# Kernel optimization log

Hardware: AMD Instinct MI355X
Metric: run time of the kernel (lower is better)

## Reference

```python
import jax, jax.numpy as jnp
import numpy as np

B, S, E, H = 2, 2048, 1024, 16
D = E // H  # head_dim = 64
EPS = 1e-6


def _angle_decay():
    # angle: 1/10000**linspace(0,1,D//2), each value repeated twice (interleaved)
    a = 1.0 / (10000.0 ** jnp.linspace(0.0, 1.0, D // 2))
    angle = jnp.repeat(a, 2)  # [D]
    decay = jnp.log(1.0 - 2.0 ** (-5.0 - jnp.arange(H, dtype=jnp.float32)))  # [H]
    return angle, decay


def _rel_pos(slen):
    angle, decay = _angle_decay()
    idx = jnp.arange(slen, dtype=jnp.float32)
    sin = jnp.sin(idx[:, None] * angle[None, :])  # [S, D]
    cos = jnp.cos(idx[:, None] * angle[None, :])  # [S, D]
    diff = idx[:, None] - idx[None, :]            # [S, S]
    tril = diff >= 0
    masked = jnp.where(tril, diff, jnp.inf)
    mask = jnp.exp(masked * decay[:, None, None])  # [H, S, S]; exp(-inf)=0 on upper tri
    mask = jnp.nan_to_num(mask)
    mask = mask / jnp.sqrt(jnp.sum(mask, axis=-1, keepdims=True))
    return sin, cos, mask


def _rotate_every_two(x):
    x1 = x[..., ::2]
    x2 = x[..., 1::2]
    return jnp.stack((-x2, x1), axis=-1).reshape(x.shape)


def _theta_shift(x, sin, cos):
    # x: [B, H, S, D]; sin/cos: [S, D] broadcast over B,H
    return x * cos + _rotate_every_two(x) * sin


def setup_inputs() -> dict:
    key = jax.random.key(0)
    ks = jax.random.split(key, 5)
    scale = 1.0 / np.sqrt(E)
    return {
        "x": jax.random.normal(ks[0], (B, S, E), dtype=jnp.float32),
        "Wq": jax.random.normal(ks[1], (E, E), dtype=jnp.float32) * scale,
        "Wk": jax.random.normal(ks[2], (E, E), dtype=jnp.float32) * scale,
        "Wv": jax.random.normal(ks[3], (E, E), dtype=jnp.float32) * scale,
        "Wg": jax.random.normal(ks[4], (E, E), dtype=jnp.float32) * scale,
    }


def reference(x, Wq, Wk, Wv, Wg):
    bsz, tgt_len, _ = x.shape
    sin, cos, mask = _rel_pos(tgt_len)
    scaling = E ** (-0.5)

    q = x @ Wq
    k = (x @ Wk) * scaling
    v = x @ Wv
    g = x @ Wg

    q = q.reshape(bsz, tgt_len, H, D).transpose(0, 2, 1, 3)  # [B,H,S,D]
    k = k.reshape(bsz, tgt_len, H, D).transpose(0, 2, 1, 3)
    vr = v.reshape(bsz, tgt_len, H, D).transpose(0, 2, 1, 3)

    qr = _theta_shift(q, sin, cos)
    kr = _theta_shift(k, sin, cos)

    qk = jnp.einsum("bhqd,bhkd->bhqk", qr, kr) * mask[None]
    denom = jax.lax.stop_gradient(
        jnp.clip(jnp.sum(jnp.abs(qk), axis=-1, keepdims=True), 1.0, 5e4)
    )
    out = jnp.einsum("bhqk,bhkd->bhqd", qk / denom, vr)
    out = out.transpose(0, 2, 1, 3)  # [B,S,H,D]

    # RMSNorm over head_dim (no affine)
    out = out * jax.lax.rsqrt(jnp.mean(out * out, axis=-1, keepdims=True) + EPS)
    out = out.reshape(bsz, tgt_len, E)
    return jax.nn.silu(g) * out
```

## Files before the change

### kernel.cpp

```cpp
#include <hip/hip_runtime.h>

typedef unsigned short u16;
typedef unsigned int u32;
typedef __attribute__((ext_vector_type(8))) __bf16 bf16x8;
typedef __attribute__((ext_vector_type(4))) float f32x4;

#define B_SZ   2
#define S_LEN  2048
#define E_DIM  1024
#define NHEAD  16
#define HD     64
#define KDIM   1024
#define NQKV   3072

__device__ __forceinline__ float bf2f(u16 u){
  union { u32 i; float f; } c; c.i = ((u32)u) << 16; return c.f;
}
__device__ __forceinline__ u16 f2bf(float f){
  union { float f; u32 i; } c; c.f = f;
  return (u16)((c.i + 0x7FFFu + ((c.i >> 16) & 1u)) >> 16);
}
__device__ __forceinline__ u16 f2bf_fast(float f){
  union { float f; u32 i; } c; c.f = f;
  return (u16)((c.i + 0x8000u) >> 16);
}
__device__ __forceinline__ void gl2lds16(const void* g, void* l){
  __builtin_amdgcn_global_load_lds((const __attribute__((address_space(1))) void*)g,
                                   (__attribute__((address_space(3))) void*)l, 16, 0, 0);
}

__global__ __launch_bounds__(256) void castx_kernel(const float* __restrict__ x, u16* __restrict__ xb){
  size_t flat = ((size_t)blockIdx.x * 256 + threadIdx.x) * 16;
  int m7 = (int)((flat >> 10) & 7);
  int cb = (int)((flat >> 3) & 7);
  size_t tile = flat & ~(size_t)63;
  float f[16];
  #pragma unroll
  for (int c = 0; c < 4; c++) *(float4*)&f[c * 4] = *(const float4*)&x[flat + c * 4];
  u16 o[16];
  #pragma unroll
  for (int i = 0; i < 16; i++) o[i] = f2bf(f[i]);
  *(uint4*)&xb[tile + ((cb ^ m7) * 8)]       = *(uint4*)&o[0];
  *(uint4*)&xb[tile + (((cb + 1) ^ m7) * 8)] = *(uint4*)&o[8];
}

__global__ __launch_bounds__(256) void wtrans_kernel(const float* __restrict__ Wq, const float* __restrict__ Wk,
                                                     const float* __restrict__ Wv, const float* __restrict__ Wg,
                                                     u16* __restrict__ WT){
  const float* Ws[4] = {Wq, Wk, Wv, Wg};
  const float* W = Ws[blockIdx.z];
  int n0 = blockIdx.x * 64, k0 = blockIdx.y * 64;
  __shared__ u16 tile[64][66];
  int t = threadIdx.x;
  int r = t >> 2, cg = (t & 3) * 16;
  const float* src = W + (size_t)(k0 + r) * E_DIM + n0 + cg;
  float f[16];
  #pragma unroll
  for (int c = 0; c < 4; c++) *(float4*)&f[c * 4] = *(const float4*)&src[c * 4];
  #pragma unroll
  for (int i = 0; i < 16; i++) tile[r][cg + i] = f2bf(f[i]);
  __syncthreads();
  u16 ov[16];
  #pragma unroll
  for (int i = 0; i < 16; i++) ov[i] = tile[cg + i][r];
  int n7 = r & 7, cb = cg >> 3;
  u16* dst = WT + (size_t)(blockIdx.z * E_DIM + n0 + r) * KDIM + k0;
  *(uint4*)&dst[(cb ^ n7) * 8]       = *(uint4*)&ov[0];
  *(uint4*)&dst[((cb + 1) ^ n7) * 8] = *(uint4*)&ov[8];
}

__global__ __launch_bounds__(256) void gemm_kernel(const u16* __restrict__ A, const u16* __restrict__ Bt,
                                                   u16* __restrict__ qkv, u16* __restrict__ gc){
  __shared__ __align__(16) u16 As[128 * 64];
  __shared__ __align__(16) u16 Bs[128 * 64];
  int m0 = blockIdx.y * 128, n0 = blockIdx.x * 128;
  int t = threadIdx.x;
  int wave = t >> 6, lane = t & 63;
  int l15 = lane & 15, quad = lane >> 4, h8 = lane & 7;
  int r0 = (wave & 1) * 64, c0 = (wave >> 1) * 64;
  f32x4 acc[4][4];
  #pragma unroll
  for (int i = 0; i < 4; i++)
    #pragma unroll
    for (int j = 0; j < 4; j++) acc[i][j] = (f32x4){0.f, 0.f, 0.f, 0.f};

  for (int k0 = 0; k0 < KDIM; k0 += 64){
    __syncthreads();
    #pragma unroll
    for (int c = 0; c < 4; c++){
      int L = c * 256 + t;
      gl2lds16(A + (size_t)(m0 + (L >> 3)) * KDIM + k0 + (L & 7) * 8, &As[L * 8]);
    }
    #pragma unroll
    for (int c = 0; c < 4; c++){
      int L = c * 256 + t;
      gl2lds16(Bt + (size_t)(n0 + (L >> 3)) * KDIM + k0 + (L & 7) * 8, &Bs[L * 8]);
    }
    __syncthreads();
    #pragma unroll
    for (int kk = 0; kk < 2; kk++){
      bf16x8 a[4], b[4];
      #pragma unroll
      for (int i = 0; i < 4; i++) a[i] = *(const bf16x8*)&As[(r0 + i * 16 + l15) * 64 + ((kk * 4 + quad) ^ h8) * 8];
      #pragma unroll
      for (int j = 0; j < 4; j++) b[j] = *(const bf16x8*)&Bs[(c0 + j * 16 + l15) * 64 + ((kk * 4 + quad) ^ h8) * 8];
      #pragma unroll
      for (int i = 0; i < 4; i++)
        #pragma unroll
        for (int j = 0; j < 4; j++)
          acc[i][j] = __builtin_amdgcn_mfma_f32_16x16x32_bf16(a[i], b[j], acc[i][j], 0, 0, 0);
    }
  }
  if (n0 < 3072){
    #pragma unroll
    for (int i = 0; i < 4; i++){
      int row = m0 + r0 + i * 16 + quad * 4;
      #pragma unroll
      for (int j = 0; j < 4; j++){
        int col = n0 + c0 + j * 16 + l15;
        #pragma unroll
        for (int r = 0; r < 4; r++)
          qkv[(size_t)(row + r) * NQKV + col] = f2bf(acc[i][j][r]);
      }
    }
  } else {
    #pragma unroll
    for (int i = 0; i < 4; i++){
      int row = m0 + r0 + i * 16 + quad * 4;
      #pragma unroll
      for (int j = 0; j < 4; j++){
        int e = (n0 - 3072) + c0 + j * 16 + l15;
        #pragma unroll
        for (int r = 0; r < 4; r++)
          gc[(size_t)(row + r) * E_DIM + e] = f2bf(acc[i][j][r]);
      }
    }
  }
}

__global__ __launch_bounds__(256) void shift_kernel(const u16* __restrict__ qkv,
                                                    u16* __restrict__ qr, u16* __restrict__ kr,
                                                    u16* __restrict__ vt){
  int sb = blockIdx.x, bh = blockIdx.y;
  int s0 = sb * 64;
  int t = threadIdx.x;
  int sl = t >> 2, dg = (t & 3) * 16;
  int s = s0 + sl;
  int h = bh & 15;
  size_t token = (size_t)(bh >> 4) * S_LEN + s;
  size_t base = token * NQKV + h * HD + dg;
  u16 qv[16], kv[16], vv[16];
  *(uint4*)&qv[0] = *(const uint4*)&qkv[base];
  *(uint4*)&qv[8] = *(const uint4*)&qkv[base + 8];
  *(uint4*)&kv[0] = *(const uint4*)&qkv[base + 1024];
  *(uint4*)&kv[8] = *(const uint4*)&qkv[base + 1024 + 8];
  *(uint4*)&vv[0] = *(const uint4*)&qkv[base + 2048];
  *(uint4*)&vv[8] = *(const uint4*)&qkv[base + 2048 + 8];
  u16 qo[16], ko[16];
  #pragma unroll
  for (int i = 0; i < 8; i++){
    int dd = dg + 2 * i;
    float a = exp2f(-(float)(dd >> 1) * (13.287712379549449f / 31.0f));
    float ang = (float)s * a;
    float sn = sinf(ang), cs = cosf(ang);
    float qe = bf2f(qv[2 * i]), qd = bf2f(qv[2 * i + 1]);
    qo[2 * i]     = f2bf(qe * cs - qd * sn);
    qo[2 * i + 1] = f2bf(qd * cs + qe * sn);
    float ke = bf2f(kv[2 * i]) * 0.03125f, kd = bf2f(kv[2 * i + 1]) * 0.03125f;
    ko[2 * i]     = f2bf(ke * cs - kd * sn);
    ko[2 * i + 1] = f2bf(kd * cs + ke * sn);
  }
  size_t dsto = ((size_t)bh * S_LEN + s) * HD;
  *(uint4*)&qr[dsto + dg]     = *(uint4*)&qo[0];
  *(uint4*)&qr[dsto + dg + 8] = *(uint4*)&qo[8];
  int s7 = s & 7, cbk = dg >> 3;
  *(uint4*)&kr[dsto + ((cbk ^ s7) * 8)]       = *(uint4*)&ko[0];
  *(uint4*)&kr[dsto + (((cbk + 1) ^ s7) * 8)] = *(uint4*)&ko[8];
  __shared__ u16 vs[64][66];
  #pragma unroll
  for (int i = 0; i < 16; i++) vs[sl][dg + i] = vv[i];
  __syncthreads();
  int d = t >> 2, jg = (t & 3) * 16;
  u16 ov[16];
  #pragma unroll
  for (int i = 0; i < 16; i++) ov[i] = vs[jg + i][d];
  int d7 = d & 7, cbv = jg >> 3;
  size_t vrow = ((size_t)bh * HD + d) * S_LEN + s0;
  *(uint4*)&vt[vrow + ((cbv ^ d7) * 8)]       = *(uint4*)&ov[0];
  *(uint4*)&vt[vrow + (((cbv + 1) ^ d7) * 8)] = *(uint4*)&ov[8];
}

__global__ __launch_bounds__(256, 2) void retention_kernel(const u16* __restrict__ qr, const u16* __restrict__ kr,
                                                           const u16* __restrict__ vt,
                                                           u16* __restrict__ pO, float* __restrict__ pBa){
  int bh = blockIdx.x;
  int qb = 15 - (int)blockIdx.y;
  int z  = blockIdx.z;
  int h = bh & 15;
  int q0 = qb * 128;
  __shared__ __align__(16) u16 Ks[64 * 64];
  __shared__ __align__(16) u16 Vs[64 * 64];
  __shared__ __align__(16) u16 Ps[128 * 72];
  int t = threadIdx.x, wave = t >> 6, lane = t & 63;
  int l15 = lane & 15, quad = lane >> 4, h8 = lane & 7;

  float decay = log1pf(-exp2f(-5.0f - (float)h));
  float negd = -decay;
  float estep = __expf(64.0f * negd);

  int qsE[2], rowb[2];
  #pragma unroll
  for (int e = 0; e < 2; e++){ rowb[e] = wave * 32 + e * 16; qsE[e] = q0 + rowb[e]; }

  bf16x8 qB[2][2];
  #pragma unroll
  for (int e = 0; e < 2; e++){
    size_t qrow = ((size_t)bh * S_LEN + qsE[e] + l15) * HD;
    qB[e][0] = *(const bf16x8*)&qr[qrow + quad * 8];
    qB[e][1] = *(const bf16x8*)&qr[qrow + 32 + quad * 8];
  }

  float win_f = 11.0f / negd;
  int win_i = (win_f > 2.1e9f) ? 0x7f000000 : (int)win_f;
  int z_lo = z ? (qb + 1) : 0;
  int z_hi = z ? (2 * qb + 1) : qb;
  int kb_lo = z_lo;
  {
    int jmin = q0 - win_i;
    if (jmin > z_lo * 64){ int wlo = jmin >> 6; kb_lo = wlo > z_lo ? wlo : z_lo; }
  }
  int k0s = kb_lo * 64;

  float em1d = expm1f(decay);
  float rfE[2]; int iE[2];
  #pragma unroll
  for (int e = 0; e < 2; e++){
    int i = qsE[e] + l15;
    iE[e] = i;
    float rowsum = expm1f((float)(i + 1) * decay) / em1d;
    rfE[e] = __expf((float)(i - k0s) * decay) * rsqrtf(rowsum);
  }
  float e1 = __expf(negd);
  float c16 = __expf(negd * 16.0f);
  float cbr[4];
  cbr[0] = __expf(negd * (float)(quad * 4));
  cbr[1] = cbr[0] * e1; cbr[2] = cbr[1] * e1; cbr[3] = cbr[2] * e1;

  f32x4 o[2][4];
  #pragma unroll
  for (int e = 0; e < 2; e++)
    #pragma unroll
    for (int dt = 0; dt < 4; dt++) o[e][dt] = (f32x4){0.f, 0.f, 0.f, 0.f};
  float babs[2] = {0.f, 0.f};

  const u16* krbh = kr + (size_t)bh * S_LEN * HD;
  const u16* vtbh = vt + (size_t)bh * HD * S_LEN;

  for (int kb = kb_lo; kb <= z_hi; kb++){
    int k0 = kb * 64;
    __syncthreads();
    #pragma unroll
    for (int c = 0; c < 2; c++){
      int L = c * 256 + t;
      gl2lds16(krbh + (size_t)k0 * HD + L * 8, &Ks[L * 8]);
    }
    #pragma unroll
    for (int c = 0; c < 2; c++){
      int L = c * 256 + t;
      gl2lds16(vtbh + (size_t)(L >> 3) * S_LEN + k0 + (L & 7) * 8, &Vs[L * 8]);
    }
    __syncthreads();

    bf16x8 kA0[4], kA1[4];
    #pragma unroll
    for (int ct = 0; ct < 4; ct++){
      int rw = (ct * 16 + l15) * 64;
      kA0[ct] = *(const bf16x8*)&Ks[rw + ((quad ^ h8) * 8)];
      kA1[ct] = *(const bf16x8*)&Ks[rw + (((quad + 4) ^ h8) * 8)];
    }
    #pragma unroll
    for (int e = 0; e < 2; e++){
      int qs = qsE[e];
      if (k0 <= qs + 15 && k0 + 63 >= qs - win_i){
        bool diag = (k0 + 64 > qs);
        float cf[4] = {cbr[0], cbr[1], cbr[2], cbr[3]};
        #pragma unroll
        for (int ct = 0; ct < 4; ct++){
          f32x4 zacc = (f32x4){0.f, 0.f, 0.f, 0.f};
          zacc = __builtin_amdgcn_mfma_f32_16x16x32_bf16(kA0[ct], qB[e][0], zacc, 0, 0, 0);
          zacc = __builtin_amdgcn_mfma_f32_16x16x32_bf16(kA1[ct], qB[e][1], zacc, 0, 0, 0);
          u16 pk[4];
          #pragma unroll
          for (int r = 0; r < 4; r++){
            float p = zacc[r] * (rfE[e] * cf[r]);
            if (diag && (k0 + ct * 16 + quad * 4 + r) > iE[e]) p = 0.f;
            babs[e] += fabsf(p);
            pk[r] = f2bf_fast(p);
            cf[r] *= c16;
          }
          u32 lo = (u32)pk[0] | ((u32)pk[1] << 16);
          u32 hi = (u32)pk[2] | ((u32)pk[3] << 16);
          *(uint2*)&Ps[(rowb[e] + l15) * 72 + ct * 16 + quad * 4] = make_uint2(lo, hi);
        }
      }
    }
    #pragma unroll
    for (int e = 0; e < 2; e++){
      int qs = qsE[e];
      if (k0 <= qs + 15 && k0 + 63 >= qs - win_i){
        bf16x8 pB0 = *(const bf16x8*)&Ps[(rowb[e] + l15) * 72 + quad * 8];
        bf16x8 pB1 = *(const bf16x8*)&Ps[(rowb[e] + l15) * 72 + 32 + quad * 8];
        #pragma unroll
        for (int dt = 0; dt < 4; dt++){
          int rw = (dt * 16 + l15) * 64;
          bf16x8 vA0 = *(const bf16x8*)&Vs[rw + ((quad ^ h8) * 8)];
          bf16x8 vA1 = *(const bf16x8*)&Vs[rw + (((quad + 4) ^ h8) * 8)];
          o[e][dt] = __builtin_amdgcn_mfma_f32_16x16x32_bf16(vA0, pB0, o[e][dt], 0, 0, 0);
          o[e][dt] = __builtin_amdgcn_mfma_f32_16x16x32_bf16(vA1, pB1, o[e][dt], 0, 0, 0);
        }
      }
    }
    #pragma unroll
    for (int e = 0; e < 2; e++) rfE[e] *= estep;
  }

  size_t slot = ((size_t)bh * 16 + qb) * 2 + z;
  u16* po = pO + slot * (4 * 128 * 16);
  #pragma unroll
  for (int e = 0; e < 2; e++){
    float bsum = babs[e];
    bsum += __shfl_xor(bsum, 16);
    bsum += __shfl_xor(bsum, 32);
    if (quad == 0) pBa[slot * 128 + rowb[e] + l15] = bsum;
    #pragma unroll
    for (int dt = 0; dt < 4; dt++){
      u16 pk[4];
      #pragma unroll
      for (int r = 0; r < 4; r++) pk[r] = f2bf(o[e][dt][r]);
      *(uint2*)&po[(dt * 128 + rowb[e] + l15) * 16 + quad * 4] = *(uint2*)pk;
    }
  }
}

__global__ __launch_bounds__(128) void combine_kernel(const u16* __restrict__ pO, const float* __restrict__ pBa,
                                                      const u16* __restrict__ gc, float* __restrict__ out){
  int bh = blockIdx.x, qb = blockIdx.y;
  int b = bh >> 4, h = bh & 15;
  int i = threadIdx.x;
  int s = qb * 128 + i;
  size_t s2 = ((size_t)bh * 16 + qb) * 2;
  const u16* p0 = pO + s2 * 8192;
  const u16* p1 = p0 + 8192;
  float v[64];
  #pragma unroll
  for (int dt = 0; dt < 4; dt++){
    u16 a[16], bb[16];
    *(uint4*)&a[0]  = *(const uint4*)&p0[(dt * 128 + i) * 16];
    *(uint4*)&a[8]  = *(const uint4*)&p0[(dt * 128 + i) * 16 + 8];
    *(uint4*)&bb[0] = *(const uint4*)&p1[(dt * 128 + i) * 16];
    *(uint4*)&bb[8] = *(const uint4*)&p1[(dt * 128 + i) * 16 + 8];
    #pragma unroll
    for (int c = 0; c < 16; c++) v[dt * 16 + c] = bf2f(a[c]) + bf2f(bb[c]);
  }
  float bsum = pBa[s2 * 128 + i] + pBa[(s2 + 1) * 128 + i];
  float dinv = 1.0f / fminf(fmaxf(bsum, 1.0f), 50000.0f);
  float ssq = 0.f;
  #pragma unroll
  for (int d = 0; d < 64; d++){ v[d] *= dinv; ssq += v[d] * v[d]; }
  float rms = rsqrtf(ssq * (1.0f / 64.0f) + 1e-6f);
  size_t gbase = ((size_t)b * S_LEN + s) * E_DIM + h * HD;
  u16 gu[64];
  #pragma unroll
  for (int c = 0; c < 8; c++) *(uint4*)&gu[c * 8] = *(const uint4*)&gc[gbase + c * 8];
  float ov[64];
  #pragma unroll
  for (int d = 0; d < 64; d++){
    float gv = bf2f(gu[d]);
    float sg = gv / (1.0f + __expf(-gv));
    ov[d] = v[d] * rms * sg;
  }
  float* obase = out + ((size_t)b * S_LEN + s) * E_DIM + h * HD;
  #pragma unroll
  for (int c = 0; c < 16; c++) *(float4*)&obase[c * 4] = *(float4*)&ov[c * 4];
}

extern "C" void kernel_launch(void* const* d_in, const int* in_sizes, int n_in,
                              void* d_out, int out_size, void* d_ws, size_t ws_size,
                              hipStream_t stream){
  const float* x  = (const float*)d_in[0];
  const float* Wq = (const float*)d_in[1];
  const float* Wk = (const float*)d_in[2];
  const float* Wv = (const float*)d_in[3];
  const float* Wg = (const float*)d_in[4];
  float* out = (float*)d_out;
  char* ws = (char*)d_ws;
  u16*   xb  = (u16*)(ws);
  u16*   WT  = (u16*)(ws + (8ull  << 20));
  u16*   qkv = (u16*)(ws + (16ull << 20));
  u16*   gcp = (u16*)(ws + (40ull << 20));
  u16*   vtp = (u16*)(ws);
  u16*   qrp = (u16*)(ws + (8ull  << 20));
  u16*   pO  = (u16*)(ws + (16ull << 20));
  u16*   krp = (u16*)(ws + (48ull << 20));
  float* pBa = (float*)(ws + (56ull << 20));

  castx_kernel    <<<dim3(1024),       256, 0, stream>>>(x, xb);
  wtrans_kernel   <<<dim3(16, 16, 4),  256, 0, stream>>>(Wq, Wk, Wv, Wg, WT);
  gemm_kernel     <<<dim3(32, 32),     256, 0, stream>>>(xb, WT, qkv, gcp);
  shift_kernel    <<<dim3(32, 32),     256, 0, stream>>>(qkv, qrp, krp, vtp);
  retention_kernel<<<dim3(32, 16, 2),  256, 0, stream>>>(qrp, krp, vtp, pO, pBa);
  combine_kernel  <<<dim3(32, 16),     128, 0, stream>>>(pO, pBa, gcp, out);
}
```

Measured before the change: 192.6 us.

## Merge prep casts into one kernel and split retention key range four ways

```diff
diff --git a/kernel.cpp b/kernel.cpp
--- a/kernel.cpp
+++ b/kernel.cpp
@@ -29,44 +29,47 @@
                                    (__attribute__((address_space(3))) void*)l, 16, 0, 0);
 }
 
-__global__ __launch_bounds__(256) void castx_kernel(const float* __restrict__ x, u16* __restrict__ xb){
-  size_t flat = ((size_t)blockIdx.x * 256 + threadIdx.x) * 16;
-  int m7 = (int)((flat >> 10) & 7);
-  int cb = (int)((flat >> 3) & 7);
-  size_t tile = flat & ~(size_t)63;
-  float f[16];
-  #pragma unroll
-  for (int c = 0; c < 4; c++) *(float4*)&f[c * 4] = *(const float4*)&x[flat + c * 4];
-  u16 o[16];
-  #pragma unroll
-  for (int i = 0; i < 16; i++) o[i] = f2bf(f[i]);
-  *(uint4*)&xb[tile + ((cb ^ m7) * 8)]       = *(uint4*)&o[0];
-  *(uint4*)&xb[tile + (((cb + 1) ^ m7) * 8)] = *(uint4*)&o[8];
-}
-
-__global__ __launch_bounds__(256) void wtrans_kernel(const float* __restrict__ Wq, const float* __restrict__ Wk,
-                                                     const float* __restrict__ Wv, const float* __restrict__ Wg,
-                                                     u16* __restrict__ WT){
-  const float* Ws[4] = {Wq, Wk, Wv, Wg};
-  const float* W = Ws[blockIdx.z];
-  int n0 = blockIdx.x * 64, k0 = blockIdx.y * 64;
+__global__ __launch_bounds__(256) void prep_kernel(const float* __restrict__ x,
+                                                   const float* __restrict__ Wq, const float* __restrict__ Wk,
+                                                   const float* __restrict__ Wv, const float* __restrict__ Wg,
+                                                   u16* __restrict__ xb, u16* __restrict__ WT){
   __shared__ u16 tile[64][66];
+  int z = blockIdx.z;
   int t = threadIdx.x;
-  int r = t >> 2, cg = (t & 3) * 16;
-  const float* src = W + (size_t)(k0 + r) * E_DIM + n0 + cg;
-  float f[16];
-  #pragma unroll
-  for (int c = 0; c < 4; c++) *(float4*)&f[c * 4] = *(const float4*)&src[c * 4];
-  #pragma unroll
-  for (int i = 0; i < 16; i++) tile[r][cg + i] = f2bf(f[i]);
-  __syncthreads();
-  u16 ov[16];
-  #pragma unroll
-  for (int i = 0; i < 16; i++) ov[i] = tile[cg + i][r];
-  int n7 = r & 7, cb = cg >> 3;
-  u16* dst = WT + (size_t)(blockIdx.z * E_DIM + n0 + r) * KDIM + k0;
-  *(uint4*)&dst[(cb ^ n7) * 8]       = *(uint4*)&ov[0];
-  *(uint4*)&dst[((cb + 1) ^ n7) * 8] = *(uint4*)&ov[8];
+  if (z < 4){
+    const float* Ws[4] = {Wq, Wk, Wv, Wg};
+    const float* W = Ws[z];
+    int n0 = blockIdx.x * 64, k0 = blockIdx.y * 64;
+    int r = t >> 2, cg = (t & 3) * 16;
+    const float* src = W + (size_t)(k0 + r) * E_DIM + n0 + cg;
+    float f[16];
+    #pragma unroll
+    for (int c = 0; c < 4; c++) *(float4*)&f[c * 4] = *(const float4*)&src[c * 4];
+    #pragma unroll
+    for (int i = 0; i < 16; i++) tile[r][cg + i] = f2bf(f[i]);
+    __syncthreads();
+    u16 ov[16];
+    #pragma unroll
+    for (int i = 0; i < 16; i++) ov[i] = tile[cg + i][r];
+    int n7 = r & 7, cb = cg >> 3;
+    u16* dst = WT + (size_t)(z * E_DIM + n0 + r) * KDIM + k0;
+    *(uint4*)&dst[(cb ^ n7) * 8]       = *(uint4*)&ov[0];
+    *(uint4*)&dst[((cb + 1) ^ n7) * 8] = *(uint4*)&ov[8];
+  } else {
+    int blk = (z - 4) * 256 + blockIdx.y * 16 + blockIdx.x;
+    size_t flat = ((size_t)blk * 256 + t) * 16;
+    int m7 = (int)((flat >> 10) & 7);
+    int cb = (int)((flat >> 3) & 7);
+    size_t tl = flat & ~(size_t)63;
+    float f[16];
+    #pragma unroll
+    for (int c = 0; c < 4; c++) *(float4*)&f[c * 4] = *(const float4*)&x[flat + c * 4];
+    u16 o[16];
+    #pragma unroll
+    for (int i = 0; i < 16; i++) o[i] = f2bf(f[i]);
+    *(uint4*)&xb[tl + ((cb ^ m7) * 8)]       = *(uint4*)&o[0];
+    *(uint4*)&xb[tl + (((cb + 1) ^ m7) * 8)] = *(uint4*)&o[8];
+  }
 }
 
 __global__ __launch_bounds__(256) void gemm_kernel(const u16* __restrict__ A, const u16* __restrict__ Bt,
@@ -192,7 +195,7 @@
 
 __global__ __launch_bounds__(256, 2) void retention_kernel(const u16* __restrict__ qr, const u16* __restrict__ kr,
                                                            const u16* __restrict__ vt,
-                                                           u16* __restrict__ pO, float* __restrict__ pBa){
+                                                           u16* __restrict__ pO, u16* __restrict__ pBa){
   int bh = blockIdx.x;
   int qb = 15 - (int)blockIdx.y;
   int z  = blockIdx.z;
@@ -222,8 +225,9 @@
 
   float win_f = 11.0f / negd;
   int win_i = (win_f > 2.1e9f) ? 0x7f000000 : (int)win_f;
-  int z_lo = z ? (qb + 1) : 0;
-  int z_hi = z ? (2 * qb + 1) : qb;
+  int nk = 2 * qb + 2;
+  int z_lo = (z * nk) >> 2;
+  int z_hi = (((z + 1) * nk) >> 2) - 1;
   int kb_lo = z_lo;
   {
     int jmin = q0 - win_i;
@@ -324,14 +328,14 @@
     for (int e = 0; e < 2; e++) rfE[e] *= estep;
   }
 
-  size_t slot = ((size_t)bh * 16 + qb) * 2 + z;
+  size_t slot = ((size_t)bh * 16 + qb) * 4 + z;
   u16* po = pO + slot * (4 * 128 * 16);
   #pragma unroll
   for (int e = 0; e < 2; e++){
     float bsum = babs[e];
     bsum += __shfl_xor(bsum, 16);
     bsum += __shfl_xor(bsum, 32);
-    if (quad == 0) pBa[slot * 128 + rowb[e] + l15] = bsum;
+    if (quad == 0) pBa[slot * 128 + rowb[e] + l15] = f2bf(bsum);
     #pragma unroll
     for (int dt = 0; dt < 4; dt++){
       u16 pk[4];
@@ -342,27 +346,30 @@
   }
 }
 
-__global__ __launch_bounds__(128) void combine_kernel(const u16* __restrict__ pO, const float* __restrict__ pBa,
+__global__ __launch_bounds__(128) void combine_kernel(const u16* __restrict__ pO, const u16* __restrict__ pBa,
                                                       const u16* __restrict__ gc, float* __restrict__ out){
   int bh = blockIdx.x, qb = blockIdx.y;
   int b = bh >> 4, h = bh & 15;
   int i = threadIdx.x;
   int s = qb * 128 + i;
-  size_t s2 = ((size_t)bh * 16 + qb) * 2;
-  const u16* p0 = pO + s2 * 8192;
-  const u16* p1 = p0 + 8192;
+  size_t s4 = ((size_t)bh * 16 + qb) * 4;
   float v[64];
   #pragma unroll
-  for (int dt = 0; dt < 4; dt++){
-    u16 a[16], bb[16];
-    *(uint4*)&a[0]  = *(const uint4*)&p0[(dt * 128 + i) * 16];
-    *(uint4*)&a[8]  = *(const uint4*)&p0[(dt * 128 + i) * 16 + 8];
-    *(uint4*)&bb[0] = *(const uint4*)&p1[(dt * 128 + i) * 16];
-    *(uint4*)&bb[8] = *(const uint4*)&p1[(dt * 128 + i) * 16 + 8];
-    #pragma unroll
-    for (int c = 0; c < 16; c++) v[dt * 16 + c] = bf2f(a[c]) + bf2f(bb[c]);
-  }
-  float bsum = pBa[s2 * 128 + i] + pBa[(s2 + 1) * 128 + i];
+  for (int d = 0; d < 64; d++) v[d] = 0.f;
+  float bsum = 0.f;
+  #pragma unroll
+  for (int z = 0; z < 4; z++){
+    const u16* pz = pO + (s4 + z) * 8192;
+    #pragma unroll
+    for (int dt = 0; dt < 4; dt++){
+      u16 a[16];
+      *(uint4*)&a[0] = *(const uint4*)&pz[(dt * 128 + i) * 16];
+      *(uint4*)&a[8] = *(const uint4*)&pz[(dt * 128 + i) * 16 + 8];
+      #pragma unroll
+      for (int c = 0; c < 16; c++) v[dt * 16 + c] += bf2f(a[c]);
+    }
+    bsum += bf2f(pBa[(s4 + z) * 128 + i]);
+  }
   float dinv = 1.0f / fminf(fmaxf(bsum, 1.0f), 50000.0f);
   float ssq = 0.f;
   #pragma unroll
@@ -394,20 +401,19 @@
   const float* Wg = (const float*)d_in[4];
   float* out = (float*)d_out;
   char* ws = (char*)d_ws;
-  u16*   xb  = (u16*)(ws);
-  u16*   WT  = (u16*)(ws + (8ull  << 20));
-  u16*   qkv = (u16*)(ws + (16ull << 20));
-  u16*   gcp = (u16*)(ws + (40ull << 20));
-  u16*   vtp = (u16*)(ws);
-  u16*   qrp = (u16*)(ws + (8ull  << 20));
-  u16*   pO  = (u16*)(ws + (16ull << 20));
-  u16*   krp = (u16*)(ws + (48ull << 20));
-  float* pBa = (float*)(ws + (56ull << 20));
-
-  castx_kernel    <<<dim3(1024),       256, 0, stream>>>(x, xb);
-  wtrans_kernel   <<<dim3(16, 16, 4),  256, 0, stream>>>(Wq, Wk, Wv, Wg, WT);
+  u16* qkv = (u16*)(ws);
+  u16* pO  = (u16*)(ws);
+  u16* xb  = (u16*)(ws + (32ull << 20));
+  u16* qrp = (u16*)(ws + (32ull << 20));
+  u16* WT  = (u16*)(ws + (40ull << 20));
+  u16* krp = (u16*)(ws + (40ull << 20));
+  u16* vtp = (u16*)(ws + (48ull << 20));
+  u16* gcp = (u16*)(ws + (56ull << 20));
+  u16* pBa = (u16*)(ws + (64ull << 20));
+
+  prep_kernel     <<<dim3(16, 16, 8),  256, 0, stream>>>(x, Wq, Wk, Wv, Wg, xb, WT);
   gemm_kernel     <<<dim3(32, 32),     256, 0, stream>>>(xb, WT, qkv, gcp);
   shift_kernel    <<<dim3(32, 32),     256, 0, stream>>>(qkv, qrp, krp, vtp);
-  retention_kernel<<<dim3(32, 16, 2),  256, 0, stream>>>(qrp, krp, vtp, pO, pBa);
+  retention_kernel<<<dim3(32, 16, 4),  256, 0, stream>>>(qrp, krp, vtp, pO, pBa);
   combine_kernel  <<<dim3(32, 16),     128, 0, stream>>>(pO, pBa, gcp, out);
 }
```

Result: faster. 188.4 us (-2.2%).
